# Optimization experiments

Measured on AMD Instinct MI355X. Metric: run time of the kernel, lower is better.

Reference implementation:

```python
import jax, jax.numpy as jnp
import numpy as np

B, S, D, H, P = 2, 1024, 512, 8, 16
DH = D // H
CUT = 15.0
SCALE = DH ** -0.5


def _ln(x, g, b, eps=1e-5):
    m = x.mean(-1, keepdims=True)
    v = ((x - m) ** 2).mean(-1, keepdims=True)
    return (x - m) / jnp.sqrt(v + eps) * g + b


def setup_inputs():
    key = jax.random.key(0)
    ks = jax.random.split(key, 12)
    f32 = jnp.float32
    nrm = lambda k, sh, s: jax.random.normal(k, sh, dtype=f32) * s
    sD = 1.0 / np.sqrt(D)
    HP3 = H * P * 3
    return {
        "x": nrm(ks[0], (B, S, D), 1.0),
        "coords": nrm(ks[1], (B, S, 3), 10.0),  # ~tens of Angstroms so cutoff matters
        "Wq": nrm(ks[2], (D, D), sD),
        "Wk": nrm(ks[3], (D, D), sD),
        "Wv": nrm(ks[4], (D, D), sD),
        "Wqp": nrm(ks[5], (D, HP3), sD), "bqp": jnp.zeros((HP3,), f32),
        "Wkp": nrm(ks[6], (D, HP3), sD), "bkp": jnp.zeros((HP3,), f32),
        "Wvp": nrm(ks[7], (D, HP3), sD), "bvp": jnp.zeros((HP3,), f32),
        "Wd1": nrm(ks[8], (1, 32), 1.0), "bd1": jnp.zeros((32,), f32),
        "Wd2": nrm(ks[9], (32, H), 1.0 / np.sqrt(32)), "bd2": jnp.zeros((H,), f32),
        "Wo": nrm(ks[10], (D + HP3, D), 1.0 / np.sqrt(D + HP3)),
        "bo": jnp.zeros((D,), f32),
        "g1": jnp.ones((D,), f32), "b1": jnp.zeros((D,), f32),
        "g2": jnp.ones((D,), f32), "b2": jnp.zeros((D,), f32),
    }


def reference(x, coords, Wq, Wk, Wv, Wqp, bqp, Wkp, bkp, Wvp, bvp,
              Wd1, bd1, Wd2, bd2, Wo, bo, g1, b1, g2, b2):
    residual = x
    xn = _ln(x, g1, b1)
    q = (xn @ Wq).reshape(B, S, H, DH)
    k = (xn @ Wk).reshape(B, S, H, DH)
    v = (xn @ Wv).reshape(B, S, H, DH)
    ce = coords[:, :, None, None, :]                     # [B,S,1,1,3]
    qp = (xn @ Wqp + bqp).reshape(B, S, H, P, 3) + ce
    kp = (xn @ Wkp + bkp).reshape(B, S, H, P, 3) + ce
    vp = (xn @ Wvp + bvp).reshape(B, S, H, P, 3)
    # pairwise residue distances [B,S,S]
    dist = jnp.linalg.norm(coords[:, :, None, :] - coords[:, None, :, :], axis=-1)
    # small per-pair distance MLP -> per-head bias
    hbias = jax.nn.relu(dist[..., None] @ Wd1 + bd1) @ Wd2 + bd2   # [B,S,S,H]
    dbias = jnp.transpose(hbias, (0, 3, 1, 2))                     # [B,H,S,S]
    spatial = (dist < CUT).astype(x.dtype)[:, None, :, :]          # [B,1,S,S]
    attn = jnp.einsum("bqhd,bkhd->bhqk", q, k) * SCALE
    # -0.5*||qp_i - kp_j||^2 expanded so the [B,H,S,S,P,3] diff tensor is never built
    qn2 = jnp.transpose(jnp.sum(qp * qp, axis=(-2, -1)), (0, 2, 1))  # [B,H,Q]
    kn2 = jnp.transpose(jnp.sum(kp * kp, axis=(-2, -1)), (0, 2, 1))  # [B,H,K]
    pdot = jnp.einsum("bqhpd,bkhpd->bhqk", qp, kp)
    point = -0.5 * (qn2[..., :, None] + kn2[..., None, :] - 2.0 * pdot)
    total = attn + point + dbias
    total = total * spatial + (spatial - 1.0) * 1e9
    w = jax.nn.softmax(total, axis=-1)   # dropout is identity at inference
    af = jnp.einsum("bhqk,bkhd->bqhd", w, v).reshape(B, S, D)
    ap = jnp.einsum("bhqk,bkhpd->bqhpd", w, vp).reshape(B, S, H * P * 3)
    out = jnp.concatenate([af, ap], axis=-1) @ Wo + bo
    out = _ln(residual + out, g2, b2)
    coord_upd = jnp.mean(ap.reshape(B, S, H, P, 3), axis=(2, 3)) * 0.1
    return out, coords + coord_upd
```

## Files before the change

kernel.cpp:

```cpp
#include <hip/hip_runtime.h>
#include <math.h>

#define B_ 2
#define S_ 1024
#define D_ 512
#define H_ 8
#define P_ 16
#define DH_ 64
#define HP3_ 384
#define CONCAT_ 896
#define CUTOFF 15.0f
#define SCALE_ 0.125f
#define QT 32
#define KT 64

__device__ __forceinline__ float waveReduceSum(float v) {
#pragma unroll
    for (int o = 32; o; o >>= 1) v += __shfl_down(v, o, 64);
    return v;
}
__device__ __forceinline__ float waveReduceMax(float v) {
#pragma unroll
    for (int o = 32; o; o >>= 1) v = fmaxf(v, __shfl_down(v, o, 64));
    return v;
}

__global__ __launch_bounds__(256) void ln1_kernel(
    const float* __restrict__ x, const float* __restrict__ g,
    const float* __restrict__ b, float* __restrict__ xn) {
    const int row = blockIdx.x;
    const int t = threadIdx.x;
    const float* xr = x + row * D_;
    float x0 = xr[t], x1 = xr[t + 256];
    __shared__ float red[4];
    float s = waveReduceSum(x0 + x1);
    int lane = t & 63, wid = t >> 6;
    if (lane == 0) red[wid] = s;
    __syncthreads();
    float mean = (red[0] + red[1] + red[2] + red[3]) * (1.0f / D_);
    __syncthreads();
    float d0 = x0 - mean, d1 = x1 - mean;
    float v = waveReduceSum(d0 * d0 + d1 * d1);
    if (lane == 0) red[wid] = v;
    __syncthreads();
    float var = (red[0] + red[1] + red[2] + red[3]) * (1.0f / D_);
    float rs = rsqrtf(var + 1e-5f);
    xn[row * D_ + t]       = d0 * rs * g[t] + b[t];
    xn[row * D_ + t + 256] = d1 * rs * g[t + 256] + b[t + 256];
}

__global__ __launch_bounds__(256) void proj_kernel(
    const float* __restrict__ xn, const float* __restrict__ coords,
    const float* __restrict__ Wq, const float* __restrict__ Wk, const float* __restrict__ Wv,
    const float* __restrict__ Wqp, const float* __restrict__ bqp,
    const float* __restrict__ Wkp, const float* __restrict__ bkp,
    const float* __restrict__ Wvp, const float* __restrict__ bvp,
    float* __restrict__ q, float* __restrict__ k, float* __restrict__ v,
    float* __restrict__ qp, float* __restrict__ kp, float* __restrict__ vp) {
    const int tid = threadIdx.x;
    const int rowBase = blockIdx.y * 64;
    const int colBase = blockIdx.x * 64;

    const float* Wseg; int ldw, segBase, segId;
    if      (colBase < 512)  { Wseg = Wq;  ldw = D_;   segBase = 0;    segId = 0; }
    else if (colBase < 1024) { Wseg = Wk;  ldw = D_;   segBase = 512;  segId = 1; }
    else if (colBase < 1536) { Wseg = Wv;  ldw = D_;   segBase = 1024; segId = 2; }
    else if (colBase < 1920) { Wseg = Wqp; ldw = HP3_; segBase = 1536; segId = 3; }
    else if (colBase < 2304) { Wseg = Wkp; ldw = HP3_; segBase = 1920; segId = 4; }
    else                     { Wseg = Wvp; ldw = HP3_; segBase = 2304; segId = 5; }
    const int segc0 = colBase - segBase;

    __shared__ float As[16][65];
    __shared__ float Bs[16][64];
    const int tx = tid & 15, ty = tid >> 4;

    float acc[4][4];
#pragma unroll
    for (int i = 0; i < 4; i++)
#pragma unroll
        for (int j = 0; j < 4; j++) acc[i][j] = 0.f;

    for (int k0 = 0; k0 < D_; k0 += 16) {
#pragma unroll
        for (int i = 0; i < 4; i++) {
            int e = tid + i * 256;
            int r = e >> 4, kk = e & 15;
            As[kk][r] = xn[(rowBase + r) * D_ + k0 + kk];
            int c = e & 63, kb = e >> 6;
            Bs[kb][c] = Wseg[(k0 + kb) * ldw + segc0 + c];
        }
        __syncthreads();
#pragma unroll
        for (int kk = 0; kk < 16; kk++) {
            float a[4], bb[4];
#pragma unroll
            for (int i = 0; i < 4; i++) a[i] = As[kk][ty * 4 + i];
#pragma unroll
            for (int j = 0; j < 4; j++) bb[j] = Bs[kk][tx * 4 + j];
#pragma unroll
            for (int i = 0; i < 4; i++)
#pragma unroll
                for (int j = 0; j < 4; j++) acc[i][j] = fmaf(a[i], bb[j], acc[i][j]);
        }
        __syncthreads();
    }

#pragma unroll
    for (int i = 0; i < 4; i++) {
        int r = rowBase + ty * 4 + i;
#pragma unroll
        for (int j = 0; j < 4; j++) {
            int lc = segc0 + tx * 4 + j;
            float val = acc[i][j];
            switch (segId) {
                case 0: q[r * D_ + lc] = val; break;
                case 1: k[r * D_ + lc] = val; break;
                case 2: v[r * D_ + lc] = val; break;
                case 3: qp[r * HP3_ + lc] = val + bqp[lc] + coords[r * 3 + lc % 3]; break;
                case 4: kp[r * HP3_ + lc] = val + bkp[lc] + coords[r * 3 + lc % 3]; break;
                case 5: vp[r * HP3_ + lc] = val + bvp[lc]; break;
            }
        }
    }
}

__global__ __launch_bounds__(256) void kn2_kernel(
    const float* __restrict__ kp, float* __restrict__ kn2) {
    int idx = blockIdx.x * 256 + threadIdx.x;
    const float* p = kp + idx * 48;
    float s = 0.f;
#pragma unroll
    for (int i = 0; i < 48; i++) s = fmaf(p[i], p[i], s);
    kn2[idx] = s;
}

__global__ __launch_bounds__(256) void attn_kernel(
    const float* __restrict__ q, const float* __restrict__ k, const float* __restrict__ v,
    const float* __restrict__ qp, const float* __restrict__ kp, const float* __restrict__ vp,
    const float* __restrict__ kn2, const float* __restrict__ coords,
    const float* __restrict__ Wd1, const float* __restrict__ bd1,
    const float* __restrict__ Wd2, const float* __restrict__ bd2,
    float* __restrict__ attn_out) {
    const int qt = blockIdx.x, h = blockIdx.y, b = blockIdx.z;
    const int tid = threadIdx.x;
    const int qpair = tid >> 4;
    const int sub   = tid & 15;
    const int q0 = qpair * 2, q1 = q0 + 1;
    const int qbase = qt * QT;

    __shared__ float sQ[QT][65];
    __shared__ float sQP[QT][49];
    __shared__ float sBuf[7296];
    __shared__ float sWt[KT][33];
    __shared__ float sCq[QT * 3], sCk[KT * 3];
    __shared__ float sKn2[KT], sQn2[QT];
    __shared__ float sM[QT], sL[QT], sTm[QT];
    __shared__ float sW1[32], sB1[32], sW2h[32];

    {
        const size_t bq = (size_t)(b * S_ + qbase);
#pragma unroll
        for (int i = 0; i < 2; i++) {
            int f4 = tid + i * 256;
            int r = f4 >> 4, c = f4 & 15;
            float4 t = *(const float4*)(q + (bq + r) * D_ + h * DH_ + c * 4);
            sQ[r][c*4+0]=t.x; sQ[r][c*4+1]=t.y; sQ[r][c*4+2]=t.z; sQ[r][c*4+3]=t.w;
        }
#pragma unroll
        for (int i = 0; i < 2; i++) {
            int f4 = tid + i * 256;
            if (f4 < 384) {
                int r = f4 / 12, c = f4 % 12;
                float4 t = *(const float4*)(qp + (bq + r) * HP3_ + h * 48 + c * 4);
                sQP[r][c*4+0]=t.x; sQP[r][c*4+1]=t.y; sQP[r][c*4+2]=t.z; sQP[r][c*4+3]=t.w;
            }
        }
        if (tid < QT * 3) sCq[tid] = coords[bq * 3 + tid];
        if (tid < 32) sW1[tid] = Wd1[tid];
        else if (tid < 64) sB1[tid - 32] = bd1[tid - 32];
        else if (tid < 96) sW2h[tid - 64] = Wd2[(tid - 64) * H_ + h];
        if (tid >= 224) { int t2 = tid - 224; sM[t2] = -3.0e38f; sL[t2] = 0.f; }
    }
    __syncthreads();
    if (tid < QT) {
        float s = 0.f;
#pragma unroll
        for (int i = 0; i < 48; i++) s = fmaf(sQP[tid][i], sQP[tid][i], s);
        sQn2[tid] = s;
    }
    const float bd2h = bd2[h];

    float o0[7] = {0,0,0,0,0,0,0}, o1[7] = {0,0,0,0,0,0,0};
    const int kb = sub * 4;
    const int db = sub * 7;

    for (int kt = 0; kt < S_ / KT; kt++) {
        const int k0 = kt * KT;
        const size_t bk = (size_t)(b * S_ + k0);
#pragma unroll
        for (int i = 0; i < 4; i++) {
            int f4 = tid + i * 256;
            int r = f4 >> 4, c = f4 & 15;
            float4 t = *(const float4*)(k + (bk + r) * D_ + h * DH_ + c * 4);
            float* dst = &sBuf[r * 65 + c * 4];
            dst[0]=t.x; dst[1]=t.y; dst[2]=t.z; dst[3]=t.w;
        }
#pragma unroll
        for (int i = 0; i < 3; i++) {
            int f4 = tid + i * 256;
            int r = f4 / 12, c = f4 % 12;
            float4 t = *(const float4*)(kp + (bk + r) * HP3_ + h * 48 + c * 4);
            float* dst = &sBuf[4160 + r * 49 + c * 4];
            dst[0]=t.x; dst[1]=t.y; dst[2]=t.z; dst[3]=t.w;
        }
        if (tid < KT) sKn2[tid] = kn2[(bk + tid) * H_ + h];
        if (tid < KT * 3) sCk[tid] = coords[bk * 3 + tid];
        __syncthreads();

        float ds0[4], ds1[4];
        {
            const float qx0 = sCq[q0*3], qy0 = sCq[q0*3+1], qz0 = sCq[q0*3+2];
            const float qx1 = sCq[q1*3], qy1 = sCq[q1*3+1], qz1 = sCq[q1*3+2];
#pragma unroll
            for (int j = 0; j < 4; j++) {
                int kk = kb + j;
                float kx = sCk[kk*3], ky = sCk[kk*3+1], kz = sCk[kk*3+2];
                float dx = qx0-kx, dy = qy0-ky, dz = qz0-kz;
                ds0[j] = sqrtf(fmaf(dx,dx,fmaf(dy,dy,dz*dz)));
                dx = qx1-kx; dy = qy1-ky; dz = qz1-kz;
                ds1[j] = sqrtf(fmaf(dx,dx,fmaf(dy,dy,dz*dz)));
            }
        }
        float bias0[4], bias1[4];
#pragma unroll
        for (int j = 0; j < 4; j++) { bias0[j] = bd2h; bias1[j] = bd2h; }
#pragma unroll 4
        for (int jj = 0; jj < 32; jj++) {
            float w1 = sW1[jj], bb = sB1[jj], w2 = sW2h[jj];
#pragma unroll
            for (int j = 0; j < 4; j++) {
                float h0 = fmaf(ds0[j], w1, bb);
                float h1 = fmaf(ds1[j], w1, bb);
                bias0[j] = fmaf(fmaxf(h0, 0.f), w2, bias0[j]);
                bias1[j] = fmaf(fmaxf(h1, 0.f), w2, bias1[j]);
            }
        }
        float d0a[4] = {0,0,0,0}, d1a[4] = {0,0,0,0};
#pragma unroll 8
        for (int d = 0; d < 64; d++) {
            float a0 = sQ[q0][d], a1 = sQ[q1][d];
#pragma unroll
            for (int j = 0; j < 4; j++) {
                float bv = sBuf[(kb + j) * 65 + d];
                d0a[j] = fmaf(a0, bv, d0a[j]);
                d1a[j] = fmaf(a1, bv, d1a[j]);
            }
        }
#pragma unroll 8
        for (int d = 0; d < 48; d++) {
            float a0 = sQP[q0][d], a1 = sQP[q1][d];
#pragma unroll
            for (int j = 0; j < 4; j++) {
                float bv = sBuf[4160 + (kb + j) * 49 + d];
                bias0[j] = fmaf(a0, bv, bias0[j]);
                bias1[j] = fmaf(a1, bv, bias1[j]);
            }
        }
        const float qn20 = sQn2[q0], qn21 = sQn2[q1];
        float lg0[4], lg1[4];
#pragma unroll
        for (int j = 0; j < 4; j++) {
            float kn = sKn2[kb + j];
            float v0 = fmaf(SCALE_, d0a[j], bias0[j]) - 0.5f * (qn20 + kn);
            float v1 = fmaf(SCALE_, d1a[j], bias1[j]) - 0.5f * (qn21 + kn);
            lg0[j] = (ds0[j] < CUTOFF) ? v0 : -1e9f;
            lg1[j] = (ds1[j] < CUTOFF) ? v1 : -1e9f;
        }
        float t0 = fmaxf(fmaxf(lg0[0], lg0[1]), fmaxf(lg0[2], lg0[3]));
        float t1 = fmaxf(fmaxf(lg1[0], lg1[1]), fmaxf(lg1[2], lg1[3]));
#pragma unroll
        for (int off = 1; off < 16; off <<= 1) {
            t0 = fmaxf(t0, __shfl_xor(t0, off, 16));
            t1 = fmaxf(t1, __shfl_xor(t1, off, 16));
        }
        if (sub == 0) { sTm[q0] = t0; sTm[q1] = t1; }
        __syncthreads();
        const float m0o = sM[q0], m1o = sM[q1];
        const float nm0 = fmaxf(m0o, sTm[q0]), nm1 = fmaxf(m1o, sTm[q1]);
        const float sc0 = __expf(m0o - nm0), sc1 = __expf(m1o - nm1);
        float ps0 = 0.f, ps1 = 0.f;
#pragma unroll
        for (int j = 0; j < 4; j++) {
            float w0 = __expf(lg0[j] - nm0);
            float w1 = __expf(lg1[j] - nm1);
            sWt[kb + j][q0] = w0; sWt[kb + j][q1] = w1;
            ps0 += w0; ps1 += w1;
        }
#pragma unroll
        for (int off = 1; off < 16; off <<= 1) {
            ps0 += __shfl_xor(ps0, off, 16);
            ps1 += __shfl_xor(ps1, off, 16);
        }
        __syncthreads();
        if (sub == 0) {
            sM[q0] = nm0; sM[q1] = nm1;
            sL[q0] = sL[q0] * sc0 + ps0;
            sL[q1] = sL[q1] * sc1 + ps1;
        }
#pragma unroll
        for (int i = 0; i < 4; i++) {
            int f4 = tid + i * 256;
            int r = f4 >> 4, c = f4 & 15;
            float4 t = *(const float4*)(v + (bk + r) * D_ + h * DH_ + c * 4);
            float* dst = &sBuf[r * 113 + c * 4];
            dst[0]=t.x; dst[1]=t.y; dst[2]=t.z; dst[3]=t.w;
        }
#pragma unroll
        for (int i = 0; i < 3; i++) {
            int f4 = tid + i * 256;
            int r = f4 / 12, c = f4 % 12;
            float4 t = *(const float4*)(vp + (bk + r) * HP3_ + h * 48 + c * 4);
            float* dst = &sBuf[r * 113 + 64 + c * 4];
            dst[0]=t.x; dst[1]=t.y; dst[2]=t.z; dst[3]=t.w;
        }
        __syncthreads();
#pragma unroll
        for (int j = 0; j < 7; j++) { o0[j] *= sc0; o1[j] *= sc1; }
#pragma unroll 4
        for (int kk = 0; kk < KT; kk++) {
            float w0 = sWt[kk][q0], w1 = sWt[kk][q1];
            const float* vr = &sBuf[kk * 113 + db];
#pragma unroll
            for (int j = 0; j < 7; j++) {
                float vv = vr[j];
                o0[j] = fmaf(w0, vv, o0[j]);
                o1[j] = fmaf(w1, vv, o1[j]);
            }
        }
        __syncthreads();
    }

    const float il0 = 1.0f / sL[q0], il1 = 1.0f / sL[q1];
    const size_t r0 = (size_t)(b * S_ + qbase + q0) * CONCAT_;
    const size_t r1 = (size_t)(b * S_ + qbase + q1) * CONCAT_;
#pragma unroll
    for (int j = 0; j < 7; j++) {
        int d = db + j;
        int off = (d < 64) ? (h * 64 + d) : (512 + h * 48 + (d - 64));
        attn_out[r0 + off] = o0[j] * il0;
        attn_out[r1 + off] = o1[j] * il1;
    }
}

__global__ __launch_bounds__(256) void out_kernel(
    const float* __restrict__ attn_out, const float* __restrict__ x,
    const float* __restrict__ coords,
    const float* __restrict__ Wo, const float* __restrict__ bo,
    const float* __restrict__ g2, const float* __restrict__ b2,
    float* __restrict__ out, float* __restrict__ coords_out) {
    const int row = blockIdx.x;
    const int t = threadIdx.x;
    __shared__ float sIn[CONCAT_];
    __shared__ float red[4];
    __shared__ float credp[2][3];

    const float* ar = attn_out + (size_t)row * CONCAT_;
    sIn[t] = ar[t]; sIn[t + 256] = ar[t + 256]; sIn[t + 512] = ar[t + 512];
    if (t < 128) sIn[t + 768] = ar[t + 768];
    __syncthreads();

    float c0 = 0.f, c1 = 0.f, c2 = 0.f;
    if (t < 128) { c0 = sIn[512 + t * 3]; c1 = sIn[512 + t * 3 + 1]; c2 = sIn[512 + t * 3 + 2]; }
#pragma unroll
    for (int o = 32; o; o >>= 1) {
        c0 += __shfl_down(c0, o, 64);
        c1 += __shfl_down(c1, o, 64);
        c2 += __shfl_down(c2, o, 64);
    }
    if (t < 128 && (t & 63) == 0) {
        credp[t >> 6][0] = c0; credp[t >> 6][1] = c1; credp[t >> 6][2] = c2;
    }
    __syncthreads();
    if (t < 3) {
        float s = credp[0][t] + credp[1][t];
        coords_out[row * 3 + t] = coords[row * 3 + t] + 0.1f * s * (1.0f / 128.f);
    }

    float a0 = bo[t], a1 = bo[t + 256];
    for (int i = 0; i < CONCAT_; i++) {
        float xi = sIn[i];
        a0 = fmaf(xi, Wo[i * D_ + t], a0);
        a1 = fmaf(xi, Wo[i * D_ + t + 256], a1);
    }
    float y0 = x[(size_t)row * D_ + t] + a0;
    float y1 = x[(size_t)row * D_ + t + 256] + a1;

    float s = waveReduceSum(y0 + y1);
    int lane = t & 63, wid = t >> 6;
    if (lane == 0) red[wid] = s;
    __syncthreads();
    float mean = (red[0] + red[1] + red[2] + red[3]) * (1.0f / D_);
    __syncthreads();
    float d0 = y0 - mean, d1 = y1 - mean;
    float vv = waveReduceSum(d0 * d0 + d1 * d1);
    if (lane == 0) red[wid] = vv;
    __syncthreads();
    float var = (red[0] + red[1] + red[2] + red[3]) * (1.0f / D_);
    float rs = rsqrtf(var + 1e-5f);
    out[(size_t)row * D_ + t]       = d0 * rs * g2[t] + b2[t];
    out[(size_t)row * D_ + t + 256] = d1 * rs * g2[t + 256] + b2[t + 256];
}

extern "C" void kernel_launch(void* const* d_in, const int* in_sizes, int n_in,
                              void* d_out, int out_size, void* d_ws, size_t ws_size,
                              hipStream_t stream) {
    const float* x      = (const float*)d_in[0];
    const float* coords = (const float*)d_in[1];
    const float* Wq     = (const float*)d_in[2];
    const float* Wk     = (const float*)d_in[3];
    const float* Wv     = (const float*)d_in[4];
    const float* Wqp    = (const float*)d_in[5];
    const float* bqp    = (const float*)d_in[6];
    const float* Wkp    = (const float*)d_in[7];
    const float* bkp    = (const float*)d_in[8];
    const float* Wvp    = (const float*)d_in[9];
    const float* bvp    = (const float*)d_in[10];
    const float* Wd1    = (const float*)d_in[11];
    const float* bd1    = (const float*)d_in[12];
    const float* Wd2    = (const float*)d_in[13];
    const float* bd2    = (const float*)d_in[14];
    const float* Wo     = (const float*)d_in[15];
    const float* bo     = (const float*)d_in[16];
    const float* g1     = (const float*)d_in[17];
    const float* b1     = (const float*)d_in[18];
    const float* g2     = (const float*)d_in[19];
    const float* b2     = (const float*)d_in[20];

    float* out        = (float*)d_out;
    float* coords_out = (float*)d_out + (size_t)B_ * S_ * D_;

    float* ws = (float*)d_ws;
    const size_t NROW = (size_t)B_ * S_;
    float* xn   = ws;
    float* q    = xn   + NROW * D_;
    float* k    = q    + NROW * D_;
    float* v    = k    + NROW * D_;
    float* qp   = v    + NROW * D_;
    float* kp   = qp   + NROW * HP3_;
    float* vp   = kp   + NROW * HP3_;
    float* kn2  = vp   + NROW * HP3_;
    float* aout = kn2  + NROW * H_;

    ln1_kernel<<<NROW, 256, 0, stream>>>(x, g1, b1, xn);

    dim3 pgrid(2688 / 64, 2048 / 64);
    proj_kernel<<<pgrid, 256, 0, stream>>>(xn, coords, Wq, Wk, Wv,
                                           Wqp, bqp, Wkp, bkp, Wvp, bvp,
                                           q, k, v, qp, kp, vp);

    kn2_kernel<<<(NROW * H_) / 256, 256, 0, stream>>>(kp, kn2);

    dim3 agrid(S_ / QT, H_, B_);
    attn_kernel<<<agrid, 256, 0, stream>>>(q, k, v, qp, kp, vp, kn2, coords,
                                           Wd1, bd1, Wd2, bd2, aout);

    out_kernel<<<NROW, 256, 0, stream>>>(aout, x, coords, Wo, bo, g2, b2,
                                         out, coords_out);
}
```

Baseline: 579.3 us.

## Vectorize attention smem access and replace per-row output projection with tiled GEMM

The attention kernel now uses padded float4 shared-memory layouts. Keys are interleaved per thread (sub+16*j) and each thread accumulates 8 output columns over 14 active subs. The V/VP tile load is restructured, and launch bounds request 2 blocks per CU. The per-row output kernel, which read Wo row by row for every output row, is split into three kernels: a 64x64 tiled GEMM that adds bias and residual, a reuse of the layernorm kernel for LN2, and a small coordinate-update kernel. The aim is to cut scalar LDS traffic and redundant global reads of Wo, at the cost of extra launches and an intermediate buffer.

```diff
diff --git a/kernel.cpp b/kernel.cpp
--- a/kernel.cpp
+++ b/kernel.cpp
@@ -13,16 +13,20 @@
 #define SCALE_ 0.125f
 #define QT 32
 #define KT 64
+#define SQS 68
+#define SQPS 52
+#define SKS 68
+#define SKPS 52
+#define SVS 120
+#define SWS 68
 
 __device__ __forceinline__ float waveReduceSum(float v) {
 #pragma unroll
     for (int o = 32; o; o >>= 1) v += __shfl_down(v, o, 64);
     return v;
 }
-__device__ __forceinline__ float waveReduceMax(float v) {
-#pragma unroll
-    for (int o = 32; o; o >>= 1) v = fmaxf(v, __shfl_down(v, o, 64));
-    return v;
+__device__ __forceinline__ float dot4(float4 a, float4 b, float acc) {
+    return fmaf(a.x, b.x, fmaf(a.y, b.y, fmaf(a.z, b.z, fmaf(a.w, b.w, acc))));
 }
 
 __global__ __launch_bounds__(256) void ln1_kernel(
@@ -134,7 +138,7 @@
     kn2[idx] = s;
 }
 
-__global__ __launch_bounds__(256) void attn_kernel(
+__global__ __launch_bounds__(256, 2) void attn_kernel(
     const float* __restrict__ q, const float* __restrict__ k, const float* __restrict__ v,
     const float* __restrict__ qp, const float* __restrict__ kp, const float* __restrict__ vp,
     const float* __restrict__ kn2, const float* __restrict__ coords,
@@ -144,74 +148,66 @@
     const int qt = blockIdx.x, h = blockIdx.y, b = blockIdx.z;
     const int tid = threadIdx.x;
     const int qpair = tid >> 4;
-    const int sub   = tid & 15;
+    const int sub = tid & 15;
     const int q0 = qpair * 2, q1 = q0 + 1;
     const int qbase = qt * QT;
 
-    __shared__ float sQ[QT][65];
-    __shared__ float sQP[QT][49];
-    __shared__ float sBuf[7296];
-    __shared__ float sWt[KT][33];
+    __shared__ float sQ[QT * SQS];
+    __shared__ float sQP[QT * SQPS];
+    __shared__ float sKV[7680];
+    __shared__ float sWt[QT * SWS];
     __shared__ float sCq[QT * 3], sCk[KT * 3];
     __shared__ float sKn2[KT], sQn2[QT];
     __shared__ float sM[QT], sL[QT], sTm[QT];
     __shared__ float sW1[32], sB1[32], sW2h[32];
 
+    const size_t bq = (size_t)(b * S_ + qbase);
+#pragma unroll
+    for (int i = 0; i < 2; i++) {
+        int f4 = tid + i * 256;
+        int r = f4 >> 4, c = f4 & 15;
+        *(float4*)&sQ[r * SQS + c * 4] = *(const float4*)(q + (bq + r) * D_ + h * DH_ + c * 4);
+    }
     {
-        const size_t bq = (size_t)(b * S_ + qbase);
-#pragma unroll
-        for (int i = 0; i < 2; i++) {
-            int f4 = tid + i * 256;
-            int r = f4 >> 4, c = f4 & 15;
-            float4 t = *(const float4*)(q + (bq + r) * D_ + h * DH_ + c * 4);
-            sQ[r][c*4+0]=t.x; sQ[r][c*4+1]=t.y; sQ[r][c*4+2]=t.z; sQ[r][c*4+3]=t.w;
-        }
-#pragma unroll
-        for (int i = 0; i < 2; i++) {
-            int f4 = tid + i * 256;
-            if (f4 < 384) {
-                int r = f4 / 12, c = f4 % 12;
-                float4 t = *(const float4*)(qp + (bq + r) * HP3_ + h * 48 + c * 4);
-                sQP[r][c*4+0]=t.x; sQP[r][c*4+1]=t.y; sQP[r][c*4+2]=t.z; sQP[r][c*4+3]=t.w;
-            }
-        }
-        if (tid < QT * 3) sCq[tid] = coords[bq * 3 + tid];
-        if (tid < 32) sW1[tid] = Wd1[tid];
-        else if (tid < 64) sB1[tid - 32] = bd1[tid - 32];
-        else if (tid < 96) sW2h[tid - 64] = Wd2[(tid - 64) * H_ + h];
-        if (tid >= 224) { int t2 = tid - 224; sM[t2] = -3.0e38f; sL[t2] = 0.f; }
-    }
+        int f4 = tid;
+        int r = f4 / 12, c = f4 % 12;
+        *(float4*)&sQP[r * SQPS + c * 4] = *(const float4*)(qp + (bq + r) * HP3_ + h * 48 + c * 4);
+        if (tid < 128) {
+            int f42 = tid + 256;
+            int r2 = f42 / 12, c2 = f42 % 12;
+            *(float4*)&sQP[r2 * SQPS + c2 * 4] = *(const float4*)(qp + (bq + r2) * HP3_ + h * 48 + c2 * 4);
+        }
+    }
+    if (tid < QT * 3) sCq[tid] = coords[bq * 3 + tid];
+    if (tid >= 128 && tid < 160) sW1[tid - 128] = Wd1[tid - 128];
+    else if (tid < 192 && tid >= 160) sB1[tid - 160] = bd1[tid - 160];
+    else if (tid >= 192 && tid < 224) sW2h[tid - 192] = Wd2[(tid - 192) * H_ + h];
+    else if (tid >= 224) { int t2 = tid - 224; sM[t2] = -3.0e38f; sL[t2] = 0.f; }
     __syncthreads();
     if (tid < QT) {
         float s = 0.f;
 #pragma unroll
-        for (int i = 0; i < 48; i++) s = fmaf(sQP[tid][i], sQP[tid][i], s);
+        for (int i = 0; i < 48; i++) s = fmaf(sQP[tid * SQPS + i], sQP[tid * SQPS + i], s);
         sQn2[tid] = s;
     }
     const float bd2h = bd2[h];
 
-    float o0[7] = {0,0,0,0,0,0,0}, o1[7] = {0,0,0,0,0,0,0};
-    const int kb = sub * 4;
-    const int db = sub * 7;
+    float o0[8] = {0,0,0,0,0,0,0,0}, o1[8] = {0,0,0,0,0,0,0,0};
+    const int db = sub * 8;
 
     for (int kt = 0; kt < S_ / KT; kt++) {
-        const int k0 = kt * KT;
-        const size_t bk = (size_t)(b * S_ + k0);
+        const size_t bk = (size_t)(b * S_ + kt * KT);
 #pragma unroll
         for (int i = 0; i < 4; i++) {
             int f4 = tid + i * 256;
             int r = f4 >> 4, c = f4 & 15;
-            float4 t = *(const float4*)(k + (bk + r) * D_ + h * DH_ + c * 4);
-            float* dst = &sBuf[r * 65 + c * 4];
-            dst[0]=t.x; dst[1]=t.y; dst[2]=t.z; dst[3]=t.w;
+            *(float4*)&sKV[r * SKS + c * 4] = *(const float4*)(k + (bk + r) * D_ + h * DH_ + c * 4);
         }
 #pragma unroll
         for (int i = 0; i < 3; i++) {
             int f4 = tid + i * 256;
             int r = f4 / 12, c = f4 % 12;
-            float4 t = *(const float4*)(kp + (bk + r) * HP3_ + h * 48 + c * 4);
-            float* dst = &sBuf[4160 + r * 49 + c * 4];
-            dst[0]=t.x; dst[1]=t.y; dst[2]=t.z; dst[3]=t.w;
+            *(float4*)&sKV[4352 + r * SKPS + c * 4] = *(const float4*)(kp + (bk + r) * HP3_ + h * 48 + c * 4);
         }
         if (tid < KT) sKn2[tid] = kn2[(bk + tid) * H_ + h];
         if (tid < KT * 3) sCk[tid] = coords[bk * 3 + tid];
@@ -223,7 +219,7 @@
             const float qx1 = sCq[q1*3], qy1 = sCq[q1*3+1], qz1 = sCq[q1*3+2];
 #pragma unroll
             for (int j = 0; j < 4; j++) {
-                int kk = kb + j;
+                int kk = sub + 16 * j;
                 float kx = sCk[kk*3], ky = sCk[kk*3+1], kz = sCk[kk*3+2];
                 float dx = qx0-kx, dy = qy0-ky, dz = qz0-kz;
                 ds0[j] = sqrtf(fmaf(dx,dx,fmaf(dy,dy,dz*dz)));
@@ -246,31 +242,33 @@
             }
         }
         float d0a[4] = {0,0,0,0}, d1a[4] = {0,0,0,0};
-#pragma unroll 8
-        for (int d = 0; d < 64; d++) {
-            float a0 = sQ[q0][d], a1 = sQ[q1][d];
+#pragma unroll 4
+        for (int d4 = 0; d4 < 16; d4++) {
+            float4 a0 = *(const float4*)&sQ[q0 * SQS + d4 * 4];
+            float4 a1 = *(const float4*)&sQ[q1 * SQS + d4 * 4];
 #pragma unroll
             for (int j = 0; j < 4; j++) {
-                float bv = sBuf[(kb + j) * 65 + d];
-                d0a[j] = fmaf(a0, bv, d0a[j]);
-                d1a[j] = fmaf(a1, bv, d1a[j]);
-            }
-        }
-#pragma unroll 8
-        for (int d = 0; d < 48; d++) {
-            float a0 = sQP[q0][d], a1 = sQP[q1][d];
+                float4 bv = *(const float4*)&sKV[(sub + 16 * j) * SKS + d4 * 4];
+                d0a[j] = dot4(a0, bv, d0a[j]);
+                d1a[j] = dot4(a1, bv, d1a[j]);
+            }
+        }
+#pragma unroll 4
+        for (int d4 = 0; d4 < 12; d4++) {
+            float4 a0 = *(const float4*)&sQP[q0 * SQPS + d4 * 4];
+            float4 a1 = *(const float4*)&sQP[q1 * SQPS + d4 * 4];
 #pragma unroll
             for (int j = 0; j < 4; j++) {
-                float bv = sBuf[4160 + (kb + j) * 49 + d];
-                bias0[j] = fmaf(a0, bv, bias0[j]);
-                bias1[j] = fmaf(a1, bv, bias1[j]);
+                float4 bv = *(const float4*)&sKV[4352 + (sub + 16 * j) * SKPS + d4 * 4];
+                bias0[j] = dot4(a0, bv, bias0[j]);
+                bias1[j] = dot4(a1, bv, bias1[j]);
             }
         }
         const float qn20 = sQn2[q0], qn21 = sQn2[q1];
         float lg0[4], lg1[4];
 #pragma unroll
         for (int j = 0; j < 4; j++) {
-            float kn = sKn2[kb + j];
+            float kn = sKn2[sub + 16 * j];
             float v0 = fmaf(SCALE_, d0a[j], bias0[j]) - 0.5f * (qn20 + kn);
             float v1 = fmaf(SCALE_, d1a[j], bias1[j]) - 0.5f * (qn21 + kn);
             lg0[j] = (ds0[j] < CUTOFF) ? v0 : -1e9f;
@@ -293,7 +291,8 @@
         for (int j = 0; j < 4; j++) {
             float w0 = __expf(lg0[j] - nm0);
             float w1 = __expf(lg1[j] - nm1);
-            sWt[kb + j][q0] = w0; sWt[kb + j][q1] = w1;
+            sWt[q0 * SWS + sub + 16 * j] = w0;
+            sWt[q1 * SWS + sub + 16 * j] = w1;
             ps0 += w0; ps1 += w1;
         }
 #pragma unroll
@@ -307,108 +306,133 @@
             sL[q0] = sL[q0] * sc0 + ps0;
             sL[q1] = sL[q1] * sc1 + ps1;
         }
+        {
+            int r = tid >> 2, cb = (tid & 3) * 7;
+#pragma unroll
+            for (int i = 0; i < 7; i++) {
+                int c4 = cb + i;
+                float4 t;
+                if (c4 < 16) t = *(const float4*)(v  + (bk + r) * D_   + h * DH_ + c4 * 4);
+                else         t = *(const float4*)(vp + (bk + r) * HP3_ + h * 48  + (c4 - 16) * 4);
+                *(float4*)&sKV[r * SVS + c4 * 4] = t;
+            }
+        }
+        __syncthreads();
+        if (sub < 14) {
+#pragma unroll
+            for (int j = 0; j < 8; j++) { o0[j] *= sc0; o1[j] *= sc1; }
+            for (int kk4 = 0; kk4 < 16; kk4++) {
+                float w0a[4], w1a[4];
+                *(float4*)w0a = *(const float4*)&sWt[q0 * SWS + kk4 * 4];
+                *(float4*)w1a = *(const float4*)&sWt[q1 * SWS + kk4 * 4];
+#pragma unroll
+                for (int jj = 0; jj < 4; jj++) {
+                    int kk = kk4 * 4 + jj;
+                    float4 va = *(const float4*)&sKV[kk * SVS + db];
+                    float4 vb = *(const float4*)&sKV[kk * SVS + db + 4];
+                    o0[0] = fmaf(w0a[jj], va.x, o0[0]); o0[1] = fmaf(w0a[jj], va.y, o0[1]);
+                    o0[2] = fmaf(w0a[jj], va.z, o0[2]); o0[3] = fmaf(w0a[jj], va.w, o0[3]);
+                    o0[4] = fmaf(w0a[jj], vb.x, o0[4]); o0[5] = fmaf(w0a[jj], vb.y, o0[5]);
+                    o0[6] = fmaf(w0a[jj], vb.z, o0[6]); o0[7] = fmaf(w0a[jj], vb.w, o0[7]);
+                    o1[0] = fmaf(w1a[jj], va.x, o1[0]); o1[1] = fmaf(w1a[jj], va.y, o1[1]);
+                    o1[2] = fmaf(w1a[jj], va.z, o1[2]); o1[3] = fmaf(w1a[jj], va.w, o1[3]);
+                    o1[4] = fmaf(w1a[jj], vb.x, o1[4]); o1[5] = fmaf(w1a[jj], vb.y, o1[5]);
+                    o1[6] = fmaf(w1a[jj], vb.z, o1[6]); o1[7] = fmaf(w1a[jj], vb.w, o1[7]);
+                }
+            }
+        }
+        __syncthreads();
+    }
+
+    if (sub < 14) {
+        const float il0 = 1.0f / sL[q0], il1 = 1.0f / sL[q1];
+        const int off = (db < 64) ? (h * 64 + db) : (512 + h * 48 + (db - 64));
+        float* r0 = attn_out + (size_t)(bq + q0) * CONCAT_ + off;
+        float* r1 = attn_out + (size_t)(bq + q1) * CONCAT_ + off;
+        float4 w0a, w0b, w1a, w1b;
+        w0a.x=o0[0]*il0; w0a.y=o0[1]*il0; w0a.z=o0[2]*il0; w0a.w=o0[3]*il0;
+        w0b.x=o0[4]*il0; w0b.y=o0[5]*il0; w0b.z=o0[6]*il0; w0b.w=o0[7]*il0;
+        w1a.x=o1[0]*il1; w1a.y=o1[1]*il1; w1a.z=o1[2]*il1; w1a.w=o1[3]*il1;
+        w1b.x=o1[4]*il1; w1b.y=o1[5]*il1; w1b.z=o1[6]*il1; w1b.w=o1[7]*il1;
+        *(float4*)r0 = w0a; *(float4*)(r0 + 4) = w0b;
+        *(float4*)r1 = w1a; *(float4*)(r1 + 4) = w1b;
+    }
+}
+
+__global__ __launch_bounds__(256) void ogemm_kernel(
+    const float* __restrict__ aout, const float* __restrict__ x,
+    const float* __restrict__ Wo, const float* __restrict__ bo,
+    float* __restrict__ yres) {
+    const int tid = threadIdx.x;
+    const int rowBase = blockIdx.y * 64;
+    const int colBase = blockIdx.x * 64;
+
+    __shared__ float As[16][65];
+    __shared__ float Bs[16][64];
+    const int tx = tid & 15, ty = tid >> 4;
+
+    float acc[4][4];
+#pragma unroll
+    for (int i = 0; i < 4; i++)
+#pragma unroll
+        for (int j = 0; j < 4; j++) acc[i][j] = 0.f;
+
+    for (int k0 = 0; k0 < CONCAT_; k0 += 16) {
 #pragma unroll
         for (int i = 0; i < 4; i++) {
-            int f4 = tid + i * 256;
-            int r = f4 >> 4, c = f4 & 15;
-            float4 t = *(const float4*)(v + (bk + r) * D_ + h * DH_ + c * 4);
-            float* dst = &sBuf[r * 113 + c * 4];
-            dst[0]=t.x; dst[1]=t.y; dst[2]=t.z; dst[3]=t.w;
-        }
-#pragma unroll
-        for (int i = 0; i < 3; i++) {
-            int f4 = tid + i * 256;
-            int r = f4 / 12, c = f4 % 12;
-            float4 t = *(const float4*)(vp + (bk + r) * HP3_ + h * 48 + c * 4);
-            float* dst = &sBuf[r * 113 + 64 + c * 4];
-            dst[0]=t.x; dst[1]=t.y; dst[2]=t.z; dst[3]=t.w;
-        }
-        __syncthreads();
-#pragma unroll
-        for (int j = 0; j < 7; j++) { o0[j] *= sc0; o1[j] *= sc1; }
-#pragma unroll 4
-        for (int kk = 0; kk < KT; kk++) {
-            float w0 = sWt[kk][q0], w1 = sWt[kk][q1];
-            const float* vr = &sBuf[kk * 113 + db];
-#pragma unroll
-            for (int j = 0; j < 7; j++) {
-                float vv = vr[j];
-                o0[j] = fmaf(w0, vv, o0[j]);
-                o1[j] = fmaf(w1, vv, o1[j]);
-            }
-        }
-        __syncthreads();
-    }
-
-    const float il0 = 1.0f / sL[q0], il1 = 1.0f / sL[q1];
-    const size_t r0 = (size_t)(b * S_ + qbase + q0) * CONCAT_;
-    const size_t r1 = (size_t)(b * S_ + qbase + q1) * CONCAT_;
-#pragma unroll
-    for (int j = 0; j < 7; j++) {
-        int d = db + j;
-        int off = (d < 64) ? (h * 64 + d) : (512 + h * 48 + (d - 64));
-        attn_out[r0 + off] = o0[j] * il0;
-        attn_out[r1 + off] = o1[j] * il1;
-    }
-}
-
-__global__ __launch_bounds__(256) void out_kernel(
-    const float* __restrict__ attn_out, const float* __restrict__ x,
-    const float* __restrict__ coords,
-    const float* __restrict__ Wo, const float* __restrict__ bo,
-    const float* __restrict__ g2, const float* __restrict__ b2,
-    float* __restrict__ out, float* __restrict__ coords_out) {
+            int e = tid + i * 256;
+            int r = e >> 4, kk = e & 15;
+            As[kk][r] = aout[(size_t)(rowBase + r) * CONCAT_ + k0 + kk];
+            int c = e & 63, kb = e >> 6;
+            Bs[kb][c] = Wo[(k0 + kb) * D_ + colBase + c];
+        }
+        __syncthreads();
+#pragma unroll
+        for (int kk = 0; kk < 16; kk++) {
+            float a[4], bb[4];
+#pragma unroll
+            for (int i = 0; i < 4; i++) a[i] = As[kk][ty * 4 + i];
+#pragma unroll
+            for (int j = 0; j < 4; j++) bb[j] = Bs[kk][tx * 4 + j];
+#pragma unroll
+            for (int i = 0; i < 4; i++)
+#pragma unroll
+                for (int j = 0; j < 4; j++) acc[i][j] = fmaf(a[i], bb[j], acc[i][j]);
+        }
+        __syncthreads();
+    }
+
+#pragma unroll
+    for (int i = 0; i < 4; i++) {
+        int r = rowBase + ty * 4 + i;
+#pragma unroll
+        for (int j = 0; j < 4; j++) {
+            int lc = colBase + tx * 4 + j;
+            yres[(size_t)r * D_ + lc] = acc[i][j] + bo[lc] + x[(size_t)r * D_ + lc];
+        }
+    }
+}
+
+__global__ __launch_bounds__(64) void coord_kernel(
+    const float* __restrict__ aout, const float* __restrict__ coords,
+    float* __restrict__ coords_out) {
     const int row = blockIdx.x;
     const int t = threadIdx.x;
-    __shared__ float sIn[CONCAT_];
-    __shared__ float red[4];
-    __shared__ float credp[2][3];
-
-    const float* ar = attn_out + (size_t)row * CONCAT_;
-    sIn[t] = ar[t]; sIn[t + 256] = ar[t + 256]; sIn[t + 512] = ar[t + 512];
-    if (t < 128) sIn[t + 768] = ar[t + 768];
-    __syncthreads();
-
-    float c0 = 0.f, c1 = 0.f, c2 = 0.f;
-    if (t < 128) { c0 = sIn[512 + t * 3]; c1 = sIn[512 + t * 3 + 1]; c2 = sIn[512 + t * 3 + 2]; }
+    const float* ap = aout + (size_t)row * CONCAT_ + 512;
+    float c0 = ap[t * 3]     + ap[(t + 64) * 3];
+    float c1 = ap[t * 3 + 1] + ap[(t + 64) * 3 + 1];
+    float c2 = ap[t * 3 + 2] + ap[(t + 64) * 3 + 2];
 #pragma unroll
     for (int o = 32; o; o >>= 1) {
         c0 += __shfl_down(c0, o, 64);
         c1 += __shfl_down(c1, o, 64);
         c2 += __shfl_down(c2, o, 64);
     }
-    if (t < 128 && (t & 63) == 0) {
-        credp[t >> 6][0] = c0; credp[t >> 6][1] = c1; credp[t >> 6][2] = c2;
-    }
-    __syncthreads();
-    if (t < 3) {
-        float s = credp[0][t] + credp[1][t];
-        coords_out[row * 3 + t] = coords[row * 3 + t] + 0.1f * s * (1.0f / 128.f);
-    }
-
-    float a0 = bo[t], a1 = bo[t + 256];
-    for (int i = 0; i < CONCAT_; i++) {
-        float xi = sIn[i];
-        a0 = fmaf(xi, Wo[i * D_ + t], a0);
-        a1 = fmaf(xi, Wo[i * D_ + t + 256], a1);
-    }
-    float y0 = x[(size_t)row * D_ + t] + a0;
-    float y1 = x[(size_t)row * D_ + t + 256] + a1;
-
-    float s = waveReduceSum(y0 + y1);
-    int lane = t & 63, wid = t >> 6;
-    if (lane == 0) red[wid] = s;
-    __syncthreads();
-    float mean = (red[0] + red[1] + red[2] + red[3]) * (1.0f / D_);
-    __syncthreads();
-    float d0 = y0 - mean, d1 = y1 - mean;
-    float vv = waveReduceSum(d0 * d0 + d1 * d1);
-    if (lane == 0) red[wid] = vv;
-    __syncthreads();
-    float var = (red[0] + red[1] + red[2] + red[3]) * (1.0f / D_);
-    float rs = rsqrtf(var + 1e-5f);
-    out[(size_t)row * D_ + t]       = d0 * rs * g2[t] + b2[t];
-    out[(size_t)row * D_ + t + 256] = d1 * rs * g2[t + 256] + b2[t + 256];
+    if (t == 0) {
+        coords_out[row * 3 + 0] = coords[row * 3 + 0] + c0 * (0.1f / 128.f);
+        coords_out[row * 3 + 1] = coords[row * 3 + 1] + c1 * (0.1f / 128.f);
+        coords_out[row * 3 + 2] = coords[row * 3 + 2] + c2 * (0.1f / 128.f);
+    }
 }
 
 extern "C" void kernel_launch(void* const* d_in, const int* in_sizes, int n_in,
@@ -464,6 +488,11 @@
     attn_kernel<<<agrid, 256, 0, stream>>>(q, k, v, qp, kp, vp, kn2, coords,
                                            Wd1, bd1, Wd2, bd2, aout);
 
-    out_kernel<<<NROW, 256, 0, stream>>>(aout, x, coords, Wo, bo, g2, b2,
-                                         out, coords_out);
-}
+    float* yres = xn;
+    dim3 ogrid(D_ / 64, 2048 / 64);
+    ogemm_kernel<<<ogrid, 256, 0, stream>>>(aout, x, Wo, bo, yres);
+
+    ln1_kernel<<<NROW, 256, 0, stream>>>(yres, g2, b2, out);
+
+    coord_kernel<<<NROW, 64, 0, stream>>>(aout, coords, coords_out);
+}
```

Measured after the change: 492.9 us. -14.9%, faster.
